# Performance work log

Measured on AMD Instinct MI355X. Metric: run time of the kernel, lower is better.

Reference implementation:

```python
import jax, jax.numpy as jnp
import numpy as np

INV_PI = 0.31830988618
PI_over_2 = 1.57079632679
PI_over_4 = 0.78539816339
N_MODES, DIM, COND_C = 8, 2, 64
LAYERS = [COND_C, 128, 512, 128, 32, N_MODES * DIM * 2 + N_MODES + 1]
N = 262144


def setup_inputs() -> dict:
    key = jax.random.key(0)
    ks = jax.random.split(key, 2 + 2 * (len(LAYERS) - 1))
    inp = {}
    inp["cond_vec"] = jax.random.normal(ks[0], (N, COND_C), jnp.float32)
    # uniforms in (0,1), bounded away from 0/1 so log/div are finite
    inp["randseed"] = jax.random.uniform(ks[1], (N, 2), jnp.float32, 1e-4, 1.0 - 1e-4)
    for i in range(len(LAYERS) - 1):
        inp[f"W{i}"] = jax.random.normal(ks[2 + 2 * i], (LAYERS[i], LAYERS[i + 1]), jnp.float32) * 0.01
        inp[f"b{i}"] = jnp.zeros((LAYERS[i + 1],), jnp.float32)
    return inp


def _mlp(x, Ws, bs):
    for i, (W, b) in enumerate(zip(Ws, bs)):
        x = x @ W + b
        if i < len(Ws) - 1:
            x = jax.nn.relu(x)
    return x


def _forward(cond_vec, randseed, Ws, bs):
    nm, d = N_MODES, DIM
    h = _mlp(cond_vec, Ws, bs)  # [N, nm*d*2 + nm + 1]
    loc = h[:, : nm * d].reshape(-1, nm, d)
    log_scale = h[:, nm * d : 2 * nm * d].reshape(-1, nm, d)
    w = jnp.abs(h[:, 2 * nm * d :])
    w = w / jnp.sum(w, axis=1, keepdims=True)  # [N, nm+1]
    wL = w[:, -1]

    r0, r1 = randseed[:, 0], randseed[:, 1]
    lambert_mask = r0 < wL
    gauss_mask = ~lambert_mask
    # in-place rescale of randseed column 0 in the torch code
    u0 = jnp.where(lambert_mask, r0 / wL, (r0 - wL) / (1.0 - wL))

    # --- gauss branch (Box-Muller) ---
    U1 = jnp.where(gauss_mask, u0, 0.5)  # masked positions: safe dummy
    U1 = jnp.maximum(U1, 1e-12)
    R = jnp.sqrt(-2.0 * jnp.log(U1))
    th = 2.0 * jnp.pi * r1
    eps_ = jnp.stack([R * jnp.cos(th), R * jnp.sin(th)], axis=-1)  # [N, 2]
    scale_sample = jnp.sum(jnp.exp(log_scale), axis=1)  # [N, 2]
    loc_sample = jnp.sum(loc, axis=1)  # [N, 2]
    z_gauss = eps_ * scale_sample + loc_sample

    # --- lambert branch (concentric disk map) ---
    wo0 = u0 * 2.0 - 1.0
    wo1 = r1 * 2.0 - 1.0
    nonzero = ~((wo0 == 0) & (wo1 == 0))
    cond1 = (jnp.abs(wo0) > jnp.abs(wo1)) & nonzero
    cond2 = (~cond1) & nonzero
    safe0 = jnp.where(wo0 == 0, 1.0, wo0)
    safe1 = jnp.where(wo1 == 0, 1.0, wo1)
    phi = jnp.where(cond1, PI_over_4 * wo1 / safe0, PI_over_2 - PI_over_4 * wo0 / safe1)
    r = jnp.where(cond1, wo0, jnp.where(cond2, wo1, 0.0))
    z_lambert = jnp.stack([r * jnp.cos(phi), r * jnp.sin(phi)], axis=-1)

    z = jnp.where(lambert_mask[:, None], z_lambert, z_gauss)  # [N, 2]

    # --- mixture log prob ---
    eps = (z[:, None, :] - loc) / jnp.exp(log_scale)  # [N, nm, 2]
    log_p = (-0.5 * d * jnp.log(2.0 * jnp.pi)
             + jnp.log(w[:, :-1] + 1e-5)
             - 0.5 * jnp.sum(eps ** 2, axis=2)
             - jnp.sum(log_scale, axis=2))  # [N, nm]
    pdf = jnp.where(z[:, 0] ** 2 + z[:, 1] ** 2 > 1.0, 0.0, INV_PI)
    lambert_log_p = jnp.log(pdf + 1e-5) + jnp.log(wL)
    log_p = jnp.concatenate([log_p, lambert_log_p[:, None]], axis=-1)  # [N, nm+1]
    return z, jax.scipy.special.logsumexp(log_p, axis=1)


def reference(cond_vec, randseed, W0, b0, W1, b1, W2, b2, W3, b3, W4, b4):
    Ws = [W0, W1, W2, W3, W4]
    bs = [b0, b1, b2, b3, b4]
    return _forward(cond_vec, randseed, Ws, bs)
```

## Files before the change

### kernel.cpp

```cpp
#include <hip/hip_runtime.h>
#include <math.h>

#define NTOT 262144
#define BROWS 64
#define THREADS 512
#define PITCH 140

typedef short bf16x8 __attribute__((ext_vector_type(8)));
typedef float f32x16 __attribute__((ext_vector_type(16)));

#define O0H 0
#define O0L 8192
#define O1H 16384
#define O1L 81920
#define O2H 147456
#define O2L 212992
#define GCNT_OFF 557056
#define GLIST_OFF 557120

__device__ __forceinline__ unsigned short bf16_rne(float x){
    unsigned u = __float_as_uint(x);
    return (unsigned short)((u + 0x7FFFu + ((u >> 16) & 1u)) >> 16);
}
__device__ __forceinline__ void split2(float x, unsigned short& h, unsigned short& l){
    h = bf16_rne(x);
    float xh = __uint_as_float(((unsigned)h) << 16);
    l = bf16_rne(x - xh);
}

__device__ __forceinline__ int frag_off(int n, int k, int nks){
    return ((((n >> 5) * nks + (k >> 4)) << 9) | (((k >> 3) & 1) << 8) | ((n & 31) << 3) | (k & 7));
}

__global__ void prep_weights(const float* __restrict__ W0, const float* __restrict__ W1,
                             const float* __restrict__ W2, unsigned short* __restrict__ ws){
    int i = blockIdx.x * 256 + threadIdx.x;
    float v; int oh, ol;
    if (i < 8192){
        int n = i >> 6, k = i & 63; v = W0[k*128 + n];
        int o = frag_off(n, k, 4);  oh = O0H + o; ol = O0L + o;
    } else if (i < 73728){
        int j = i - 8192; int n = j >> 7, k = j & 127; v = W1[k*512 + n];
        int o = frag_off(n, k, 8);  oh = O1H + o; ol = O1L + o;
    } else if (i < 139264){
        int j = i - 73728; int n = j >> 9, k = j & 511; v = W2[k*128 + n];
        int o = frag_off(n, k, 32); oh = O2H + o; ol = O2L + o;
    } else return;
    unsigned short h, l; split2(v, h, l);
    ws[oh] = h; ws[ol] = l;
}

__device__ __forceinline__ void epilogue_row(const float* __restrict__ h, float r0v, float r1v,
        float& z0o, float& z1o, float& lseo, float& wLo, float& u0o, bool& lamo){
    float wraw[9]; float wsum = 0.0f;
    #pragma unroll
    for (int j = 0; j < 9; ++j){ wraw[j] = fabsf(h[32 + j]); wsum += wraw[j]; }
    float wL = wraw[8] / wsum;
    const bool lambert = r0v < wL;
    float u0 = lambert ? (r0v / wL) : ((r0v - wL) / (1.0f - wL));
    float U1 = lambert ? 0.5f : u0;
    U1 = fmaxf(U1, 1e-12f);
    float R  = sqrtf(-2.0f * logf(U1));
    float th = 6.28318530717958647692f * r1v;
    float ce = cosf(th), se = sinf(th);
    float es0[8], es1[8];
    float ssum0 = 0.0f, ssum1 = 0.0f, lsum0 = 0.0f, lsum1 = 0.0f;
    #pragma unroll
    for (int m = 0; m < 8; ++m){
        es0[m] = expf(h[16 + 2*m]); es1[m] = expf(h[16 + 2*m + 1]);
        ssum0 += es0[m]; ssum1 += es1[m];
        lsum0 += h[2*m]; lsum1 += h[2*m + 1];
    }
    float zg0 = (R * ce) * ssum0 + lsum0;
    float zg1 = (R * se) * ssum1 + lsum1;
    float wo0 = u0 * 2.0f - 1.0f;
    float wo1 = r1v * 2.0f - 1.0f;
    bool nonzero = !((wo0 == 0.0f) && (wo1 == 0.0f));
    bool c1 = (fabsf(wo0) > fabsf(wo1)) && nonzero;
    bool c2 = (!c1) && nonzero;
    float sa0 = (wo0 == 0.0f) ? 1.0f : wo0;
    float sa1 = (wo1 == 0.0f) ? 1.0f : wo1;
    float phi = c1 ? (0.78539816339f * wo1 / sa0)
                   : (1.57079632679f - 0.78539816339f * wo0 / sa1);
    float rr = c1 ? wo0 : (c2 ? wo1 : 0.0f);
    float zl0 = rr * cosf(phi);
    float zl1 = rr * sinf(phi);
    float z0 = lambert ? zl0 : zg0;
    float z1 = lambert ? zl1 : zg1;
    float lp[9];
    #pragma unroll
    for (int m = 0; m < 8; ++m){
        float e0 = (z0 - h[2*m])     / es0[m];
        float e1 = (z1 - h[2*m + 1]) / es1[m];
        float wm = wraw[m] / wsum;
        lp[m] = (-1.83787706640934548356f + logf(wm + 1e-5f))
                - 0.5f * (e0*e0 + e1*e1)
                - (h[16 + 2*m] + h[16 + 2*m + 1]);
    }
    float pdf = (z0*z0 + z1*z1 > 1.0f) ? 0.0f : 0.31830988618f;
    lp[8] = logf(pdf + 1e-5f) + logf(wL);
    float mx = lp[0];
    #pragma unroll
    for (int j = 1; j < 9; ++j) mx = fmaxf(mx, lp[j]);
    float s = 0.0f;
    #pragma unroll
    for (int j = 0; j < 9; ++j) s += expf(lp[j] - mx);
    z0o = z0; z1o = z1; lseo = mx + logf(s); wLo = wL; u0o = u0; lamo = lambert;
}

__device__ __forceinline__ f32x16 bias_init(const float* __restrict__ b, int mt, int lane, int nmax){
    f32x16 c;
    const int hq = ((lane >> 5) << 2);
    #pragma unroll
    for (int r = 0; r < 16; ++r){
        int n = mt + (r & 3) + ((r >> 2) << 3) + hq;
        c[r] = (n < nmax) ? b[n] : 0.0f;
    }
    return c;
}

__device__ __forceinline__ void write_tile(unsigned short* __restrict__ ah, unsigned short* __restrict__ al,
        int brow, int m0, int lane, const f32x16 acc, bool relu){
    const int hq = ((lane >> 5) << 2);
    #pragma unroll
    for (int q = 0; q < 4; ++q){
        ushort4 vh, vl;
        #pragma unroll
        for (int r = 0; r < 4; ++r){
            float x = acc[q*4 + r];
            if (relu) x = fmaxf(x, 0.0f);
            unsigned short hh, ll; split2(x, hh, ll);
            (&vh.x)[r] = hh; (&vl.x)[r] = ll;
        }
        const int off = brow*PITCH + m0 + q*8 + hq;
        *(ushort4*)(ah + off) = vh;
        *(ushort4*)(al + off) = vl;
    }
}

__device__ __forceinline__ void write_tile_f32t(float* __restrict__ dst,
        int brow, int m0, int lane, const f32x16 acc){
    const int hq = ((lane >> 5) << 2);
    #pragma unroll
    for (int q = 0; q < 4; ++q){
        #pragma unroll
        for (int r = 0; r < 4; ++r){
            int n = m0 + q*8 + hq + r;
            dst[n*64 + brow] = fmaxf(acc[q*4 + r], 0.0f);
        }
    }
}

template<int NK>
__device__ __forceinline__ void gemm_phase(
        const unsigned short* __restrict__ wh_base, const unsigned short* __restrict__ wl_base,
        const unsigned short* __restrict__ acth, const unsigned short* __restrict__ actl,
        int brow, int lane, f32x16& acc){
    const int kl = ((lane >> 5) << 3);
    #pragma unroll 2
    for (int ks = 0; ks < NK; ++ks){
        const int k0 = ks*16 + kl;
        bf16x8 ah = *(const bf16x8*)(acth + brow*PITCH + k0);
        bf16x8 al = *(const bf16x8*)(actl + brow*PITCH + k0);
        bf16x8 wh = *(const bf16x8*)(wh_base + ks*512 + lane*8);
        bf16x8 wl = *(const bf16x8*)(wl_base + ks*512 + lane*8);
        acc = __builtin_amdgcn_mfma_f32_32x32x16_bf16(wh, ah, acc, 0, 0, 0);
        acc = __builtin_amdgcn_mfma_f32_32x32x16_bf16(wh, al, acc, 0, 0, 0);
        acc = __builtin_amdgcn_mfma_f32_32x32x16_bf16(wl, ah, acc, 0, 0, 0);
    }
}

__global__ __launch_bounds__(THREADS, 4)
void gmm_mfma(const float* __restrict__ cond, const float* __restrict__ rnd,
              const unsigned short* __restrict__ ws,
              const float* __restrict__ b0, const float* __restrict__ b1,
              const float* __restrict__ b2,
              const float* __restrict__ W3, const float* __restrict__ b3,
              const float* __restrict__ W4, const float* __restrict__ b4,
              int* __restrict__ gcnt, int* __restrict__ glist,
              float* __restrict__ out)
{
    extern __shared__ unsigned char smem[];
    unsigned short* aAh = (unsigned short*)smem;
    unsigned short* aAl = aAh + 64*PITCH;
    unsigned short* aBh = aAl + 64*PITCH;
    unsigned short* aBl = aBh + 64*PITCH;
    float* h2f = (float*)smem;
    float* h3f = (float*)(smem + 35840);
    float* h4f = (float*)(smem + 44032);

    const int tid  = threadIdx.x;
    const int lane = tid & 63;
    const int wv   = tid >> 6;
    const int row0 = blockIdx.x * BROWS;
    const int rg   = wv & 1;
    const int ct   = wv >> 1;
    const int brow = rg*32 + (lane & 31);
    const int m0   = ct * 32;
    const int kl   = ((lane >> 5) << 3);

    {
        f32x16 acc0 = bias_init(b0, m0, lane, 128);
        #pragma unroll 2
        for (int ks = 0; ks < 4; ++ks){
            const int k0 = ks*16 + kl;
            const float* cp = cond + (size_t)(row0 + brow)*64 + k0;
            float4 ca = *(const float4*)cp;
            float4 cb = *(const float4*)(cp + 4);
            float xs[8] = {ca.x, ca.y, ca.z, ca.w, cb.x, cb.y, cb.z, cb.w};
            bf16x8 ah, al;
            #pragma unroll
            for (int j = 0; j < 8; ++j){
                unsigned short hh, ll; split2(xs[j], hh, ll);
                ah[j] = (short)hh; al[j] = (short)ll;
            }
            bf16x8 wh = *(const bf16x8*)(ws + O0H + (ct*4 + ks)*512 + lane*8);
            bf16x8 wl = *(const bf16x8*)(ws + O0L + (ct*4 + ks)*512 + lane*8);
            acc0 = __builtin_amdgcn_mfma_f32_32x32x16_bf16(wh, ah, acc0, 0, 0, 0);
            acc0 = __builtin_amdgcn_mfma_f32_32x32x16_bf16(wh, al, acc0, 0, 0, 0);
            acc0 = __builtin_amdgcn_mfma_f32_32x32x16_bf16(wl, ah, acc0, 0, 0, 0);
        }
        write_tile(aAh, aAl, brow, m0, lane, acc0, true);
    }
    __syncthreads();

    f32x16 acc2 = bias_init(b2, m0, lane, 128);
    for (int c = 0; c < 4; ++c){
        f32x16 a1 = bias_init(b1 + c*128, m0, lane, 128);
        gemm_phase<8>(ws + O1H + (size_t)((c*4 + ct)*8)*512, ws + O1L + (size_t)((c*4 + ct)*8)*512,
                      aAh, aAl, brow, lane, a1);
        __syncthreads();
        write_tile(aBh, aBl, brow, m0, lane, a1, true);
        __syncthreads();
        gemm_phase<8>(ws + O2H + (size_t)(ct*32 + c*8)*512, ws + O2L + (size_t)(ct*32 + c*8)*512,
                      aBh, aBl, brow, lane, acc2);
    }
    __syncthreads();
    write_tile_f32t(h2f, brow, m0, lane, acc2);
    __syncthreads();

    {
        const int row = tid & 63;
        const int nb  = tid >> 6;
        float acc[4];
        #pragma unroll
        for (int c = 0; c < 4; ++c) acc[c] = b3[nb*4 + c];
        #pragma unroll 8
        for (int k = 0; k < 128; ++k){
            float a = h2f[k*64 + row];
            const float* wr = W3 + k*32 + nb*4;
            #pragma unroll
            for (int c = 0; c < 4; ++c) acc[c] = fmaf(a, wr[c], acc[c]);
        }
        #pragma unroll
        for (int c = 0; c < 4; ++c) h3f[(nb*4 + c)*64 + row] = fmaxf(acc[c], 0.0f);
    }
    __syncthreads();

    {
        const int row = tid & 63;
        const int nb  = tid >> 6;
        float acc[6];
        #pragma unroll
        for (int c = 0; c < 6; ++c){ int n = nb*6 + c; acc[c] = (n < 41) ? b4[n] : 0.0f; }
        #pragma unroll 8
        for (int k = 0; k < 32; ++k){
            float a = h3f[k*64 + row];
            const float* wr = W4 + k*41;
            #pragma unroll
            for (int c = 0; c < 6; ++c){ int n = nb*6 + c; if (n < 41) acc[c] = fmaf(a, wr[n], acc[c]); }
        }
        #pragma unroll
        for (int c = 0; c < 6; ++c){ int n = nb*6 + c; if (n < 41) h4f[n*64 + row] = acc[c]; }
    }
    __syncthreads();

    if (tid < 64){
        const int row  = tid;
        const int grow = row0 + row;
        float h[41];
        #pragma unroll
        for (int j = 0; j < 41; ++j) h[j] = h4f[j*64 + row];
        float2 rv = *(const float2*)(rnd + 2*(size_t)grow);
        float z0, z1, lse, wL, u0; bool lam;
        epilogue_row(h, rv.x, rv.y, z0, z1, lse, wL, u0, lam);
        ((float2*)out)[grow] = make_float2(z0, z1);
        out[(size_t)2*NTOT + grow] = lse;
        bool flag = (fabsf(rv.x - wL) < 5e-3f)
                 || (wL < 3e-3f) || (wL > 0.5f)
                 || (fabsf(z0*z0 + z1*z1 - 1.0f) < (lam ? 0.02f : 0.2f))
                 || (!lam && u0 < 3e-3f);
        if (flag){ int idx = atomicAdd(gcnt, 1); glist[idx] = grow; }
    }
}

__global__ __launch_bounds__(512, 2)
void gmm_fix(const float* __restrict__ cond, const float* __restrict__ rnd,
             const float* __restrict__ W0, const float* __restrict__ b0,
             const float* __restrict__ W1, const float* __restrict__ b1,
             const float* __restrict__ W2, const float* __restrict__ b2,
             const float* __restrict__ W3, const float* __restrict__ b3,
             const float* __restrict__ W4, const float* __restrict__ b4,
             const int* __restrict__ gcnt, const int* __restrict__ glist,
             float* __restrict__ out)
{
    __shared__ float fb[7296];
    float* c0g = fb;
    float* f0g = fb + 512;
    float* f1g = fb + 1536;
    float* f2g = fb + 5632;
    float* f3g = fb + 6656;
    float* h4g = fb + 6912;
    const int tid = threadIdx.x;
    const int nflag = *gcnt;

    for (int base = blockIdx.x * 8; base < nflag; base += gridDim.x * 8){
        const int g = min(8, nflag - base);
        {
            int i = tid >> 6, k = tid & 63;
            if (i < g) c0g[i*64 + k] = cond[(size_t)glist[base + i]*64 + k];
        }
        __syncthreads();
        if (tid < 128){
            float acc[8];
            #pragma unroll
            for (int i = 0; i < 8; ++i) acc[i] = b0[tid];
            #pragma unroll 8
            for (int k = 0; k < 64; ++k){
                float w = W0[k*128 + tid];
                #pragma unroll
                for (int i = 0; i < 8; ++i) acc[i] = fmaf(c0g[i*64 + k], w, acc[i]);
            }
            for (int i = 0; i < g; ++i) f0g[i*128 + tid] = fmaxf(acc[i], 0.0f);
        }
        __syncthreads();
        {
            float acc[8];
            #pragma unroll
            for (int i = 0; i < 8; ++i) acc[i] = b1[tid];
            #pragma unroll 8
            for (int k = 0; k < 128; ++k){
                float w = W1[k*512 + tid];
                #pragma unroll
                for (int i = 0; i < 8; ++i) acc[i] = fmaf(f0g[i*128 + k], w, acc[i]);
            }
            for (int i = 0; i < g; ++i) f1g[i*512 + tid] = fmaxf(acc[i], 0.0f);
        }
        __syncthreads();
        if (tid < 128){
            float acc[8];
            #pragma unroll
            for (int i = 0; i < 8; ++i) acc[i] = b2[tid];
            #pragma unroll 8
            for (int k = 0; k < 512; ++k){
                float w = W2[k*128 + tid];
                #pragma unroll
                for (int i = 0; i < 8; ++i) acc[i] = fmaf(f1g[i*512 + k], w, acc[i]);
            }
            for (int i = 0; i < g; ++i) f2g[i*128 + tid] = fmaxf(acc[i], 0.0f);
        }
        __syncthreads();
        if (tid < 32){
            float acc[8];
            #pragma unroll
            for (int i = 0; i < 8; ++i) acc[i] = b3[tid];
            #pragma unroll 8
            for (int k = 0; k < 128; ++k){
                float w = W3[k*32 + tid];
                #pragma unroll
                for (int i = 0; i < 8; ++i) acc[i] = fmaf(f2g[i*128 + k], w, acc[i]);
            }
            for (int i = 0; i < g; ++i) f3g[i*32 + tid] = fmaxf(acc[i], 0.0f);
        }
        __syncthreads();
        if (tid < 41){
            float acc[8];
            #pragma unroll
            for (int i = 0; i < 8; ++i) acc[i] = b4[tid];
            #pragma unroll 8
            for (int k = 0; k < 32; ++k){
                float w = W4[k*41 + tid];
                #pragma unroll
                for (int i = 0; i < 8; ++i) acc[i] = fmaf(f3g[i*32 + k], w, acc[i]);
            }
            for (int i = 0; i < g; ++i) h4g[i*48 + tid] = acc[i];
        }
        __syncthreads();
        if (tid < g){
            const int grow = glist[base + tid];
            float2 rv = *(const float2*)(rnd + 2*(size_t)grow);
            float z0, z1, lse, wL, u0; bool lam;
            epilogue_row(&h4g[tid*48], rv.x, rv.y, z0, z1, lse, wL, u0, lam);
            ((float2*)out)[grow] = make_float2(z0, z1);
            out[(size_t)2*NTOT + grow] = lse;
        }
        __syncthreads();
    }
}

extern "C" void kernel_launch(void* const* d_in, const int* in_sizes, int n_in,
                              void* d_out, int out_size, void* d_ws, size_t ws_size,
                              hipStream_t stream) {
    const float* cond = (const float*)d_in[0];
    const float* rnd  = (const float*)d_in[1];
    const float* W0 = (const float*)d_in[2];  const float* b0 = (const float*)d_in[3];
    const float* W1 = (const float*)d_in[4];  const float* b1 = (const float*)d_in[5];
    const float* W2 = (const float*)d_in[6];  const float* b2 = (const float*)d_in[7];
    const float* W3 = (const float*)d_in[8];  const float* b3 = (const float*)d_in[9];
    const float* W4 = (const float*)d_in[10]; const float* b4 = (const float*)d_in[11];
    float* out = (float*)d_out;
    unsigned short* ws = (unsigned short*)d_ws;
    int* gcnt  = (int*)((char*)d_ws + GCNT_OFF);
    int* glist = (int*)((char*)d_ws + GLIST_OFF);

    hipMemsetAsync(gcnt, 0, 4, stream);
    hipLaunchKernelGGL(prep_weights, dim3(544), dim3(256), 0, stream, W0, W1, W2, ws);

    hipLaunchKernelGGL(gmm_mfma, dim3(NTOT / BROWS), dim3(THREADS), 71680, stream,
                       cond, rnd, ws, b0, b1, b2, W3, b3, W4, b4, gcnt, glist, out);

    hipLaunchKernelGGL(gmm_fix, dim3(256), dim3(512), 0, stream,
                       cond, rnd, W0, b0, W1, b1, W2, b2, W3, b3, W4, b4, gcnt, glist, out);
}
```

Before: 854.5 us.

## Split per-row epilogue into separate full-parallel kernel via global h4 buffer

When the workspace is large enough, the MLP kernel writes its final-layer outputs (41 columns per row) to a column-major global buffer instead of running the epilogue on only 64 of 512 threads. A new kernel then runs the epilogue with one thread per row across all threads. This removes the serialized single-wave tail from the main kernel, at the cost of writing and re-reading about 43 MB of intermediates and an extra launch. The fix-up kernel grid is also raised from 256 to 1024 blocks.

Result: slower. 897.1 us (+5.0%).

```diff
diff --git a/kernel.cpp b/kernel.cpp
--- a/kernel.cpp
+++ b/kernel.cpp
@@ -17,6 +17,8 @@
 #define O2L 212992
 #define GCNT_OFF 557056
 #define GLIST_OFF 557120
+#define H4_OFF 2097152
+#define WS_NEED (H4_OFF + (size_t)41 * NTOT * 4)
 
 __device__ __forceinline__ unsigned short bf16_rne(float x){
     unsigned u = __float_as_uint(x);
@@ -108,6 +110,13 @@
     z0o = z0; z1o = z1; lseo = mx + logf(s); wLo = wL; u0o = u0; lamo = lambert;
 }
 
+__device__ __forceinline__ bool flag_row(float r0v, float z0, float z1, float wL, float u0, bool lam){
+    return (fabsf(r0v - wL) < 5e-3f)
+        || (wL < 3e-3f) || (wL > 0.5f)
+        || (fabsf(z0*z0 + z1*z1 - 1.0f) < (lam ? 0.02f : 0.2f))
+        || (!lam && u0 < 3e-3f);
+}
+
 __device__ __forceinline__ f32x16 bias_init(const float* __restrict__ b, int mt, int lane, int nmax){
     f32x16 c;
     const int hq = ((lane >> 5) << 2);
@@ -151,14 +160,13 @@
     }
 }
 
-template<int NK>
-__device__ __forceinline__ void gemm_phase(
+__device__ __forceinline__ void gemm_phase8(
         const unsigned short* __restrict__ wh_base, const unsigned short* __restrict__ wl_base,
         const unsigned short* __restrict__ acth, const unsigned short* __restrict__ actl,
         int brow, int lane, f32x16& acc){
     const int kl = ((lane >> 5) << 3);
     #pragma unroll 2
-    for (int ks = 0; ks < NK; ++ks){
+    for (int ks = 0; ks < 8; ++ks){
         const int k0 = ks*16 + kl;
         bf16x8 ah = *(const bf16x8*)(acth + brow*PITCH + k0);
         bf16x8 al = *(const bf16x8*)(actl + brow*PITCH + k0);
@@ -170,6 +178,7 @@
     }
 }
 
+template<int WITH_EPI>
 __global__ __launch_bounds__(THREADS, 4)
 void gmm_mfma(const float* __restrict__ cond, const float* __restrict__ rnd,
               const unsigned short* __restrict__ ws,
@@ -178,6 +187,7 @@
               const float* __restrict__ W3, const float* __restrict__ b3,
               const float* __restrict__ W4, const float* __restrict__ b4,
               int* __restrict__ gcnt, int* __restrict__ glist,
+              float* __restrict__ h4g,
               float* __restrict__ out)
 {
     extern __shared__ unsigned char smem[];
@@ -227,13 +237,13 @@
     f32x16 acc2 = bias_init(b2, m0, lane, 128);
     for (int c = 0; c < 4; ++c){
         f32x16 a1 = bias_init(b1 + c*128, m0, lane, 128);
-        gemm_phase<8>(ws + O1H + (size_t)((c*4 + ct)*8)*512, ws + O1L + (size_t)((c*4 + ct)*8)*512,
-                      aAh, aAl, brow, lane, a1);
+        gemm_phase8(ws + O1H + (size_t)((c*4 + ct)*8)*512, ws + O1L + (size_t)((c*4 + ct)*8)*512,
+                    aAh, aAl, brow, lane, a1);
         __syncthreads();
         write_tile(aBh, aBl, brow, m0, lane, a1, true);
         __syncthreads();
-        gemm_phase<8>(ws + O2H + (size_t)(ct*32 + c*8)*512, ws + O2L + (size_t)(ct*32 + c*8)*512,
-                      aBh, aBl, brow, lane, acc2);
+        gemm_phase8(ws + O2H + (size_t)(ct*32 + c*8)*512, ws + O2L + (size_t)(ct*32 + c*8)*512,
+                    aBh, aBl, brow, lane, acc2);
     }
     __syncthreads();
     write_tile_f32t(h2f, brow, m0, lane, acc2);
@@ -275,22 +285,45 @@
     }
     __syncthreads();
 
-    if (tid < 64){
-        const int row  = tid;
-        const int grow = row0 + row;
-        float h[41];
-        #pragma unroll
-        for (int j = 0; j < 41; ++j) h[j] = h4f[j*64 + row];
-        float2 rv = *(const float2*)(rnd + 2*(size_t)grow);
-        float z0, z1, lse, wL, u0; bool lam;
-        epilogue_row(h, rv.x, rv.y, z0, z1, lse, wL, u0, lam);
-        ((float2*)out)[grow] = make_float2(z0, z1);
-        out[(size_t)2*NTOT + grow] = lse;
-        bool flag = (fabsf(rv.x - wL) < 5e-3f)
-                 || (wL < 3e-3f) || (wL > 0.5f)
-                 || (fabsf(z0*z0 + z1*z1 - 1.0f) < (lam ? 0.02f : 0.2f))
-                 || (!lam && u0 < 3e-3f);
-        if (flag){ int idx = atomicAdd(gcnt, 1); glist[idx] = grow; }
+    if (WITH_EPI){
+        if (tid < 64){
+            const int row  = tid;
+            const int grow = row0 + row;
+            float h[41];
+            #pragma unroll
+            for (int j = 0; j < 41; ++j) h[j] = h4f[j*64 + row];
+            float2 rv = *(const float2*)(rnd + 2*(size_t)grow);
+            float z0, z1, lse, wL, u0; bool lam;
+            epilogue_row(h, rv.x, rv.y, z0, z1, lse, wL, u0, lam);
+            ((float2*)out)[grow] = make_float2(z0, z1);
+            out[(size_t)2*NTOT + grow] = lse;
+            if (flag_row(rv.x, z0, z1, wL, u0, lam)){
+                int idx = atomicAdd(gcnt, 1); glist[idx] = grow;
+            }
+        }
+    } else {
+        for (int idx = tid; idx < 41*64; idx += THREADS){
+            int n = idx >> 6, r = idx & 63;
+            h4g[(size_t)n*NTOT + row0 + r] = h4f[n*64 + r];
+        }
+    }
+}
+
+__global__ void gmm_epi(const float* __restrict__ rnd, const float* __restrict__ h4g,
+                        int* __restrict__ gcnt, int* __restrict__ glist,
+                        float* __restrict__ out)
+{
+    const int grow = blockIdx.x * 256 + threadIdx.x;
+    float h[41];
+    #pragma unroll
+    for (int j = 0; j < 41; ++j) h[j] = h4g[(size_t)j*NTOT + grow];
+    float2 rv = *(const float2*)(rnd + 2*(size_t)grow);
+    float z0, z1, lse, wL, u0; bool lam;
+    epilogue_row(h, rv.x, rv.y, z0, z1, lse, wL, u0, lam);
+    ((float2*)out)[grow] = make_float2(z0, z1);
+    out[(size_t)2*NTOT + grow] = lse;
+    if (flag_row(rv.x, z0, z1, wL, u0, lam)){
+        int idx = atomicAdd(gcnt, 1); glist[idx] = grow;
     }
 }
 
@@ -412,13 +445,21 @@
     unsigned short* ws = (unsigned short*)d_ws;
     int* gcnt  = (int*)((char*)d_ws + GCNT_OFF);
     int* glist = (int*)((char*)d_ws + GLIST_OFF);
+    float* h4g = (float*)((char*)d_ws + H4_OFF);
 
     hipMemsetAsync(gcnt, 0, 4, stream);
     hipLaunchKernelGGL(prep_weights, dim3(544), dim3(256), 0, stream, W0, W1, W2, ws);
 
-    hipLaunchKernelGGL(gmm_mfma, dim3(NTOT / BROWS), dim3(THREADS), 71680, stream,
-                       cond, rnd, ws, b0, b1, b2, W3, b3, W4, b4, gcnt, glist, out);
-
-    hipLaunchKernelGGL(gmm_fix, dim3(256), dim3(512), 0, stream,
+    if (ws_size >= WS_NEED){
+        hipLaunchKernelGGL(gmm_mfma<0>, dim3(NTOT / BROWS), dim3(THREADS), 71680, stream,
+                           cond, rnd, ws, b0, b1, b2, W3, b3, W4, b4, gcnt, glist, h4g, out);
+        hipLaunchKernelGGL(gmm_epi, dim3(NTOT / 256), dim3(256), 0, stream,
+                           rnd, h4g, gcnt, glist, out);
+    } else {
+        hipLaunchKernelGGL(gmm_mfma<1>, dim3(NTOT / BROWS), dim3(THREADS), 71680, stream,
+                           cond, rnd, ws, b0, b1, b2, W3, b3, W4, b4, gcnt, glist, h4g, out);
+    }
+
+    hipLaunchKernelGGL(gmm_fix, dim3(1024), dim3(512), 0, stream,
                        cond, rnd, W0, b0, W1, b1, W2, b2, W3, b3, W4, b4, gcnt, glist, out);
 }
```

## Software-pipeline weight fragment loads across MFMA phases and use LDS-only barriers

Applied to the files above, without the earlier changes.

Splits the layer-1/layer-2 MFMA loops into half-steps and prefetches the next half's global weight fragments into registers while the current half issues MFMAs, double-buffered across the chunk loop. Replaces __syncthreads with a barrier that waits only on LDS counters, so in-flight global weight loads can cross the barrier. Also raises the fix-up kernel grid from 256 to 1024 blocks. The prefetching increases register pressure under launch bounds of 4 blocks per CU and risks spills. The custom barrier relies on correct manual ordering of LDS accesses.

After: 864.2 us. About the same (+1.1%).

```diff
diff --git a/kernel.cpp b/kernel.cpp
--- a/kernel.cpp
+++ b/kernel.cpp
@@ -17,6 +17,8 @@
 #define O2L 212992
 #define GCNT_OFF 557056
 #define GLIST_OFF 557120
+
+#define SOFTBAR() asm volatile("s_waitcnt lgkmcnt(0)\n\ts_barrier" ::: "memory")
 
 __device__ __forceinline__ unsigned short bf16_rne(float x){
     unsigned u = __float_as_uint(x);
@@ -108,6 +110,13 @@
     z0o = z0; z1o = z1; lseo = mx + logf(s); wLo = wL; u0o = u0; lamo = lambert;
 }
 
+__device__ __forceinline__ bool flag_row(float r0v, float z0, float z1, float wL, float u0, bool lam){
+    return (fabsf(r0v - wL) < 5e-3f)
+        || (wL < 3e-3f) || (wL > 0.5f)
+        || (fabsf(z0*z0 + z1*z1 - 1.0f) < (lam ? 0.02f : 0.2f))
+        || (!lam && u0 < 3e-3f);
+}
+
 __device__ __forceinline__ f32x16 bias_init(const float* __restrict__ b, int mt, int lane, int nmax){
     f32x16 c;
     const int hq = ((lane >> 5) << 2);
@@ -151,22 +160,28 @@
     }
 }
 
-template<int NK>
-__device__ __forceinline__ void gemm_phase(
-        const unsigned short* __restrict__ wh_base, const unsigned short* __restrict__ wl_base,
+__device__ __forceinline__ void load_half(const unsigned short* __restrict__ bh,
+                                          const unsigned short* __restrict__ bl,
+                                          int ks0, int lane, bf16x8* wh, bf16x8* wl){
+    #pragma unroll
+    for (int i = 0; i < 4; ++i){
+        wh[i] = *(const bf16x8*)(bh + (ks0 + i)*512 + lane*8);
+        wl[i] = *(const bf16x8*)(bl + (ks0 + i)*512 + lane*8);
+    }
+}
+
+__device__ __forceinline__ void mfma_half(const bf16x8* wh, const bf16x8* wl,
         const unsigned short* __restrict__ acth, const unsigned short* __restrict__ actl,
-        int brow, int lane, f32x16& acc){
+        int ks0, int brow, int lane, f32x16& acc){
     const int kl = ((lane >> 5) << 3);
-    #pragma unroll 2
-    for (int ks = 0; ks < NK; ++ks){
-        const int k0 = ks*16 + kl;
+    #pragma unroll
+    for (int i = 0; i < 4; ++i){
+        const int k0 = (ks0 + i)*16 + kl;
         bf16x8 ah = *(const bf16x8*)(acth + brow*PITCH + k0);
         bf16x8 al = *(const bf16x8*)(actl + brow*PITCH + k0);
-        bf16x8 wh = *(const bf16x8*)(wh_base + ks*512 + lane*8);
-        bf16x8 wl = *(const bf16x8*)(wl_base + ks*512 + lane*8);
-        acc = __builtin_amdgcn_mfma_f32_32x32x16_bf16(wh, ah, acc, 0, 0, 0);
-        acc = __builtin_amdgcn_mfma_f32_32x32x16_bf16(wh, al, acc, 0, 0, 0);
-        acc = __builtin_amdgcn_mfma_f32_32x32x16_bf16(wl, ah, acc, 0, 0, 0);
+        acc = __builtin_amdgcn_mfma_f32_32x32x16_bf16(wh[i], ah, acc, 0, 0, 0);
+        acc = __builtin_amdgcn_mfma_f32_32x32x16_bf16(wh[i], al, acc, 0, 0, 0);
+        acc = __builtin_amdgcn_mfma_f32_32x32x16_bf16(wl[i], ah, acc, 0, 0, 0);
     }
 }
 
@@ -199,6 +214,8 @@
     const int m0   = ct * 32;
     const int kl   = ((lane >> 5) << 3);
 
+    bf16x8 whA[4], wlA[4], whB[4], wlB[4];
+
     {
         f32x16 acc0 = bias_init(b0, m0, lane, 128);
         #pragma unroll 2
@@ -222,22 +239,32 @@
         }
         write_tile(aAh, aAl, brow, m0, lane, acc0, true);
     }
-    __syncthreads();
+    load_half(ws + O1H + (size_t)(ct*8)*512, ws + O1L + (size_t)(ct*8)*512, 0, lane, whA, wlA);
+    SOFTBAR();
 
     f32x16 acc2 = bias_init(b2, m0, lane, 128);
     for (int c = 0; c < 4; ++c){
+        const unsigned short* b1h = ws + O1H + (size_t)((c*4 + ct)*8)*512;
+        const unsigned short* b1l = ws + O1L + (size_t)((c*4 + ct)*8)*512;
+        const unsigned short* b2h = ws + O2H + (size_t)(ct*32 + c*8)*512;
+        const unsigned short* b2l = ws + O2L + (size_t)(ct*32 + c*8)*512;
         f32x16 a1 = bias_init(b1 + c*128, m0, lane, 128);
-        gemm_phase<8>(ws + O1H + (size_t)((c*4 + ct)*8)*512, ws + O1L + (size_t)((c*4 + ct)*8)*512,
-                      aAh, aAl, brow, lane, a1);
-        __syncthreads();
+        load_half(b1h, b1l, 4, lane, whB, wlB);
+        mfma_half(whA, wlA, aAh, aAl, 0, brow, lane, a1);
+        load_half(b2h, b2l, 0, lane, whA, wlA);
+        mfma_half(whB, wlB, aAh, aAl, 4, brow, lane, a1);
+        load_half(b2h, b2l, 4, lane, whB, wlB);
+        SOFTBAR();
         write_tile(aBh, aBl, brow, m0, lane, a1, true);
-        __syncthreads();
-        gemm_phase<8>(ws + O2H + (size_t)(ct*32 + c*8)*512, ws + O2L + (size_t)(ct*32 + c*8)*512,
-                      aBh, aBl, brow, lane, acc2);
-    }
-    __syncthreads();
+        SOFTBAR();
+        mfma_half(whA, wlA, aBh, aBl, 0, brow, lane, acc2);
+        if (c < 3)
+            load_half(ws + O1H + (size_t)(((c+1)*4 + ct)*8)*512,
+                      ws + O1L + (size_t)(((c+1)*4 + ct)*8)*512, 0, lane, whA, wlA);
+        mfma_half(whB, wlB, aBh, aBl, 4, brow, lane, acc2);
+    }
     write_tile_f32t(h2f, brow, m0, lane, acc2);
-    __syncthreads();
+    SOFTBAR();
 
     {
         const int row = tid & 63;
@@ -252,10 +279,11 @@
             #pragma unroll
             for (int c = 0; c < 4; ++c) acc[c] = fmaf(a, wr[c], acc[c]);
         }
+        SOFTBAR();
         #pragma unroll
         for (int c = 0; c < 4; ++c) h3f[(nb*4 + c)*64 + row] = fmaxf(acc[c], 0.0f);
     }
-    __syncthreads();
+    SOFTBAR();
 
     {
         const int row = tid & 63;
@@ -273,7 +301,7 @@
         #pragma unroll
         for (int c = 0; c < 6; ++c){ int n = nb*6 + c; if (n < 41) h4f[n*64 + row] = acc[c]; }
     }
-    __syncthreads();
+    SOFTBAR();
 
     if (tid < 64){
         const int row  = tid;
@@ -286,11 +314,9 @@
         epilogue_row(h, rv.x, rv.y, z0, z1, lse, wL, u0, lam);
         ((float2*)out)[grow] = make_float2(z0, z1);
         out[(size_t)2*NTOT + grow] = lse;
-        bool flag = (fabsf(rv.x - wL) < 5e-3f)
-                 || (wL < 3e-3f) || (wL > 0.5f)
-                 || (fabsf(z0*z0 + z1*z1 - 1.0f) < (lam ? 0.02f : 0.2f))
-                 || (!lam && u0 < 3e-3f);
-        if (flag){ int idx = atomicAdd(gcnt, 1); glist[idx] = grow; }
+        if (flag_row(rv.x, z0, z1, wL, u0, lam)){
+            int idx = atomicAdd(gcnt, 1); glist[idx] = grow;
+        }
     }
 }
 
@@ -419,6 +445,6 @@
     hipLaunchKernelGGL(gmm_mfma, dim3(NTOT / BROWS), dim3(THREADS), 71680, stream,
                        cond, rnd, ws, b0, b1, b2, W3, b3, W4, b4, gcnt, glist, out);
 
-    hipLaunchKernelGGL(gmm_fix, dim3(256), dim3(512), 0, stream,
+    hipLaunchKernelGGL(gmm_fix, dim3(1024), dim3(512), 0, stream,
                        cond, rnd, W0, b0, W1, b1, W2, b2, W3, b3, W4, b4, gcnt, glist, out);
 }
```
